# Kernel optimization log

Measured on AMD Instinct MI355X. Metric: run time of the kernel, lower is better.

Reference implementation:

```python
import jax, jax.numpy as jnp
import numpy as np

B, Q, C, K = 2, 300, 80, 300
MH = MW = 128
TH = TW = 320


def setup_inputs() -> dict:
    key = jax.random.key(0)
    k1, k2, k3 = jax.random.split(key, 3)
    pred_logits = jax.random.normal(k1, (B, Q, C), dtype=jnp.float32)
    pred_boxes = jax.random.uniform(k2, (B, Q, 4), dtype=jnp.float32)  # cxcywh in [0,1]
    pred_masks = jax.random.normal(k3, (B, Q, MH, MW), dtype=jnp.float32)
    # fixed target size so resize output shape is static (original uses .item() per image)
    orig_target_sizes = jnp.full((B, 2), 320.0, dtype=jnp.float32)  # (w, h)
    return {
        'pred_logits': pred_logits,
        'pred_boxes': pred_boxes,
        'pred_masks': pred_masks,
        'orig_target_sizes': orig_target_sizes,
        'target_h': TH,
        'target_w': TW,
    }


def reference(pred_logits, pred_boxes, pred_masks, orig_target_sizes, target_h, target_w):
    b, q, c = pred_logits.shape
    # cxcywh -> xyxy
    cx, cy, w, h = jnp.split(pred_boxes, 4, axis=-1)
    boxes_xyxy = jnp.concatenate([cx - 0.5 * w, cy - 0.5 * h, cx + 0.5 * w, cy + 0.5 * h], axis=-1)
    # scale factor [w, h, w, h] per image
    scale_fct = jnp.concatenate([orig_target_sizes, orig_target_sizes], axis=1)[:, None, :]  # [B,1,4]
    boxes_abs = boxes_xyxy * scale_fct  # [B,Q,4]

    # focal-loss path: sigmoid scores, topk over flattened (query, class)
    scores_flat = jax.nn.sigmoid(pred_logits).reshape(b, q * c)
    scores, index_flat = jax.lax.top_k(scores_flat, K)  # [B,K]
    labels = index_flat % c
    query_indices = index_flat // c  # [B,K]

    top_boxes = jnp.take_along_axis(boxes_abs, query_indices[:, :, None], axis=1)  # [B,K,4]
    top_masks = jnp.take_along_axis(pred_masks, query_indices[:, :, None, None], axis=1)  # [B,K,MH,MW]

    # bilinear resize, half-pixel centers == torch align_corners=False
    resized = jax.image.resize(top_masks, (b, K, target_h, target_w), method='linear')
    binary_masks = (jax.nn.sigmoid(resized) > 0.5).astype(jnp.float32)

    return scores, labels, top_boxes, binary_masks
```

## Files before the change

kernel.cpp:

```cpp
#include <hip/hip_runtime.h>
#include <stdint.h>

constexpr int Bq = 2;
constexpr int Qn = 300;
constexpr int Cn = 80;
constexpr int Kn = 300;
constexpr int NFLAT = Qn * Cn;
constexpr int MHs = 128;
constexpr int MWs = 128;
constexpr int THs = 320;
constexpr int TWs = 320;

constexpr int OFF_SCORES = 0;
constexpr int OFF_LABELS = Bq * Kn;
constexpr int OFF_BOXES  = 2 * Bq * Kn;
constexpr int OFF_MASKS  = 2 * Bq * Kn + Bq * Kn * 4;

constexpr int TPB = 1024;
constexpr int EPT = (NFLAT + TPB - 1) / TPB;

typedef float vf4  __attribute__((ext_vector_type(4)));
typedef float uvf4 __attribute__((ext_vector_type(4), aligned(4)));

__global__ __launch_bounds__(TPB) void topk_kernel(
    const float* __restrict__ logits,
    const float* __restrict__ boxes,
    const float* __restrict__ osz,
    float* __restrict__ out,
    int* __restrict__ qidx_ws)
{
    const int b   = blockIdx.x;
    const int tid = threadIdx.x;
    const float* lg = logits + (size_t)b * NFLAT;

    uint32_t key[EPT];
    #pragma unroll
    for (int j = 0; j < EPT; ++j) {
        int idx = j * TPB + tid;
        bool valid = (idx < NFLAT);
        float x = valid ? lg[idx] : 0.0f;
        float s = 1.0f / (1.0f + expf(-x));
        key[j] = valid ? __float_as_uint(s) : 0u;
    }

    __shared__ uint32_t sh_lo, sh_hi;
    __shared__ int sh_cnt, sh_done;
    __shared__ unsigned long long sk[1024];

    if (tid == 0) { sh_lo = 0u; sh_hi = 0xFFFFFFFFu; sh_cnt = 0; sh_done = 0; }
    __syncthreads();

    for (int it = 0; it < 32; ++it) {
        if (sh_done) break;
        uint32_t lo = sh_lo, hi = sh_hi;
        if (hi - lo <= 1) break;
        uint32_t mid = lo + ((hi - lo) >> 1);
        int c = 0;
        #pragma unroll
        for (int j = 0; j < EPT; ++j) c += (key[j] > mid) ? 1 : 0;
        for (int off = 32; off > 0; off >>= 1) c += __shfl_down(c, off);
        if ((tid & 63) == 0 && c) atomicAdd(&sh_cnt, c);
        __syncthreads();
        if (tid == 0) {
            int total = sh_cnt;
            sh_cnt = 0;
            if (total >= Kn) { sh_lo = mid; if (total <= 768) sh_done = 1; }
            else             { sh_hi = mid; }
        }
        __syncthreads();
    }

    const uint32_t T = sh_lo;
    #pragma unroll
    for (int j = 0; j < EPT; ++j) {
        int idx = j * TPB + tid;
        if (idx < NFLAT && key[j] > T) {
            int p = atomicAdd(&sh_cnt, 1);
            if (p < 1024)
                sk[p] = ((unsigned long long)key[j] << 32)
                      | (unsigned long long)(0xFFFFFFFFu - (uint32_t)idx);
        }
    }
    __syncthreads();

    const int n = min(sh_cnt, 1024);
    if (tid < n) {
        unsigned long long my = sk[tid];
        int rank = 0;
        for (int i = 0; i < n; ++i) rank += (sk[i] > my) ? 1 : 0;
        if (rank < Kn) {
            uint32_t idx = 0xFFFFFFFFu - (uint32_t)(my & 0xFFFFFFFFull);
            float score  = __uint_as_float((uint32_t)(my >> 32));
            int label = (int)(idx % (uint32_t)Cn);
            int q     = (int)(idx / (uint32_t)Cn);

            out[OFF_SCORES + b * Kn + rank] = score;
            out[OFF_LABELS + b * Kn + rank] = (float)label;

            const float sw = osz[b * 2 + 0];
            const float sh = osz[b * 2 + 1];
            const float* bx = boxes + ((size_t)(b * Qn + q)) * 4;
            float cx = bx[0], cy = bx[1], w = bx[2], h = bx[3];
            float* ob = out + OFF_BOXES + ((size_t)(b * Kn + rank)) * 4;
            ob[0] = (cx - 0.5f * w) * sw;
            ob[1] = (cy - 0.5f * h) * sh;
            ob[2] = (cx + 0.5f * w) * sw;
            ob[3] = (cy + 0.5f * h) * sh;

            qidx_ws[b * Kn + rank] = q;
        }
    }
}

__global__ __launch_bounds__(320) void resize_kernel(
    const float* __restrict__ masks,
    const int* __restrict__ qidx_ws,
    float* __restrict__ out)
{
    const int blk = blockIdx.x;
    const int bk  = blk >> 2;
    const int s   = blk & 3;
    const int tid = threadIdx.x;
    const int b   = bk / Kn;
    const int q   = qidx_ws[bk];
    const int c   = tid % 80;
    const int rs  = tid / 80;

    const float* M = masks + ((size_t)(b * Qn + q)) * (MHs * MWs);

    int s0;
    {
        float sx0 = fmaf(0.4f, (float)(4 * c), -0.3f);
        int i0 = (int)floorf(sx0);
        s0 = min(max(i0, 0), MWs - 4);
    }
    float W[4][4];
    #pragma unroll
    for (int t = 0; t < 4; ++t) {
        int ox = 4 * c + t;
        float sx = fmaf(0.4f, (float)ox, -0.3f);
        int ix0 = (int)floorf(sx);
        float fr = sx - (float)ix0;
        int ca = max(ix0, 0);
        int cb = min(ix0 + 1, MWs - 1);
        float wa = 1.0f - fr, wb = fr;
        #pragma unroll
        for (int j = 0; j < 4; ++j) {
            float w = 0.0f;
            if (s0 + j == ca) w += wa;
            if (s0 + j == cb) w += wb;
            W[t][j] = w;
        }
    }

    auto hrow = [&](float* hv, int r) {
        uvf4 a = *(const uvf4*)(M + r * MWs + s0);
        #pragma unroll
        for (int t = 0; t < 4; ++t)
            hv[t] = fmaf(W[t][0], a[0],
                    fmaf(W[t][1], a[1],
                    fmaf(W[t][2], a[2], W[t][3] * a[3])));
    };

    float* outm = out + OFF_MASKS + (size_t)bk * (THs * TWs);
    auto emit = [&](int row, float wA, const float* pA, float wB, const float* pB) {
        vf4 o;
        #pragma unroll
        for (int t = 0; t < 4; ++t) {
            float v = fmaf(wA, pA[t], wB * pB[t]);
            o[t] = (v > 0.0f) ? 1.0f : 0.0f;
        }
        __builtin_nontemporal_store(o, (vf4*)(outm + (size_t)row * TWs + 4 * c));
    };

    const int Y0 = 80 * s + 20 * rs;
    const int M0 = Y0 / 5;

    float hA[4], hB[4], hC[4], hD[4];
    hrow(hC, max(2 * M0 - 1, 0));
    hrow(hD, 2 * M0);

    #pragma unroll
    for (int g = 0; g < 4; ++g) {
        #pragma unroll
        for (int t = 0; t < 4; ++t) { hA[t] = hC[t]; hB[t] = hD[t]; }
        const int Mg = M0 + g;
        hrow(hC, 2 * Mg + 1);
        hrow(hD, min(2 * Mg + 2, MHs - 1));

        const int Y = Y0 + 5 * g;
        emit(Y + 0, 0.3f, hA, 0.7f, hB);
        emit(Y + 1, 0.9f, hB, 0.1f, hC);
        emit(Y + 2, 0.5f, hB, 0.5f, hC);
        emit(Y + 3, 0.1f, hB, 0.9f, hC);
        emit(Y + 4, 0.7f, hC, 0.3f, hD);
    }
}

extern "C" void kernel_launch(void* const* d_in, const int* in_sizes, int n_in,
                              void* d_out, int out_size, void* d_ws, size_t ws_size,
                              hipStream_t stream) {
    const float* logits = (const float*)d_in[0];
    const float* boxes  = (const float*)d_in[1];
    const float* masks  = (const float*)d_in[2];
    const float* osz    = (const float*)d_in[3];

    float* out = (float*)d_out;
    int* qidx  = (int*)d_ws;

    topk_kernel<<<Bq, TPB, 0, stream>>>(logits, boxes, osz, out, qidx);
    resize_kernel<<<Bq * Kn * 4, 320, 0, stream>>>(masks, qidx, out);
}
```

Measured before the change: 331.4 us.

## Replace bisection top-k threshold search with single-pass logit histogram

The top-k kernel no longer bisects over sigmoid bit patterns with a barrier per iteration. It builds a 4096-bin shared-memory histogram of the raw logits over [-8, 8), runs a suffix scan to find the bin that holds the k-th element, and applies sigmoid only to the candidates at or above that bin. This cuts the per-iteration reductions and syncs and most exp calls. The risk is that a crowded bin or heavy clamping could push candidates past the 1024-slot buffer; separately, the mask stores become plain stores instead of nontemporal ones.

Measured after the change: 334.4 us. About the same (+0.9%).

```diff
diff --git a/kernel.cpp b/kernel.cpp
--- a/kernel.cpp
+++ b/kernel.cpp
@@ -33,57 +33,82 @@
     const int tid = threadIdx.x;
     const float* lg = logits + (size_t)b * NFLAT;
 
-    uint32_t key[EPT];
+    float xv[EPT];
+    short bn[EPT];
     #pragma unroll
     for (int j = 0; j < EPT; ++j) {
         int idx = j * TPB + tid;
         bool valid = (idx < NFLAT);
-        float x = valid ? lg[idx] : 0.0f;
-        float s = 1.0f / (1.0f + expf(-x));
-        key[j] = valid ? __float_as_uint(s) : 0u;
-    }
-
-    __shared__ uint32_t sh_lo, sh_hi;
-    __shared__ int sh_cnt, sh_done;
+        float x = valid ? lg[idx] : -1e30f;
+        xv[j] = x;
+        int bi = (int)floorf((x + 8.0f) * 256.0f);
+        bn[j] = (short)min(max(bi, 0), 4095);
+        if (!valid) bn[j] = -1;
+    }
+
+    __shared__ int hist[4096];
+    __shared__ int scanA[1024], scanB[1024];
     __shared__ unsigned long long sk[1024];
-
-    if (tid == 0) { sh_lo = 0u; sh_hi = 0xFFFFFFFFu; sh_cnt = 0; sh_done = 0; }
-    __syncthreads();
-
-    for (int it = 0; it < 32; ++it) {
-        if (sh_done) break;
-        uint32_t lo = sh_lo, hi = sh_hi;
-        if (hi - lo <= 1) break;
-        uint32_t mid = lo + ((hi - lo) >> 1);
-        int c = 0;
-        #pragma unroll
-        for (int j = 0; j < EPT; ++j) c += (key[j] > mid) ? 1 : 0;
-        for (int off = 32; off > 0; off >>= 1) c += __shfl_down(c, off);
-        if ((tid & 63) == 0 && c) atomicAdd(&sh_cnt, c);
+    __shared__ int s_cnt, s_seg, s_B;
+
+    {
+        int4* h4 = (int4*)hist;
+        for (int i = tid; i < 4096 / 4; i += TPB) h4[i] = make_int4(0, 0, 0, 0);
+    }
+    if (tid == 0) s_cnt = 0;
+    __syncthreads();
+
+    #pragma unroll
+    for (int j = 0; j < EPT; ++j)
+        if (bn[j] >= 0) atomicAdd(&hist[bn[j]], 1);
+    __syncthreads();
+
+    int sum = hist[4 * tid] + hist[4 * tid + 1] + hist[4 * tid + 2] + hist[4 * tid + 3];
+    scanA[tid] = sum;
+    __syncthreads();
+    int* src = scanA;
+    int* dst = scanB;
+    for (int d = 1; d < 1024; d <<= 1) {
+        int v = src[tid] + ((tid + d < 1024) ? src[tid + d] : 0);
+        dst[tid] = v;
         __syncthreads();
-        if (tid == 0) {
-            int total = sh_cnt;
-            sh_cnt = 0;
-            if (total >= Kn) { sh_lo = mid; if (total <= 768) sh_done = 1; }
-            else             { sh_hi = mid; }
-        }
-        __syncthreads();
-    }
-
-    const uint32_t T = sh_lo;
+        int* t = src; src = dst; dst = t;
+    }
+
+    int sfx  = src[tid];
+    int sfx1 = (tid < 1023) ? src[tid + 1] : 0;
+    if (sfx >= Kn && sfx1 < Kn) s_seg = tid;
+    __syncthreads();
+
+    if (tid == 0) {
+        int t = s_seg;
+        int cumAbove = (t < 1023) ? src[t + 1] : 0;
+        int B = 4 * t;
+        for (int i = 3; i >= 0; --i) {
+            int bin = 4 * t + i;
+            int c = hist[bin];
+            if (cumAbove + c >= Kn) { B = bin; break; }
+            cumAbove += c;
+        }
+        s_B = B;
+    }
+    __syncthreads();
+
+    const int Bv = s_B;
     #pragma unroll
     for (int j = 0; j < EPT; ++j) {
-        int idx = j * TPB + tid;
-        if (idx < NFLAT && key[j] > T) {
-            int p = atomicAdd(&sh_cnt, 1);
+        if ((int)bn[j] >= Bv) {
+            int idx = j * TPB + tid;
+            float s = 1.0f / (1.0f + expf(-xv[j]));
+            int p = atomicAdd(&s_cnt, 1);
             if (p < 1024)
-                sk[p] = ((unsigned long long)key[j] << 32)
+                sk[p] = ((unsigned long long)__float_as_uint(s) << 32)
                       | (unsigned long long)(0xFFFFFFFFu - (uint32_t)idx);
         }
     }
     __syncthreads();
 
-    const int n = min(sh_cnt, 1024);
+    const int n = min(s_cnt, 1024);
     if (tid < n) {
         unsigned long long my = sk[tid];
         int rank = 0;
@@ -170,7 +195,7 @@
             float v = fmaf(wA, pA[t], wB * pB[t]);
             o[t] = (v > 0.0f) ? 1.0f : 0.0f;
         }
-        __builtin_nontemporal_store(o, (vf4*)(outm + (size_t)row * TWs + 4 * c));
+        *(vf4*)(outm + (size_t)row * TWs + 4 * c) = o;
     };
 
     const int Y0 = 80 * s + 20 * rs;
```

## Split top-k into multi-block histogram, threshold, collect and rank kernels

Applied to the files above, without the earlier changes.

Replaces the single-block-per-image bisection top-k with a grid-wide pipeline. A 256-bin logit histogram is built across 47 blocks per image, a threshold bin is picked, candidates are collected by global atomics into a workspace, and a final block ranks them. The aim is to spread the serial 2-block top-k work across many CUs, at the cost of four extra launches plus a memset. The fixed logit-range binning risks more than 1024 candidates, which would silently truncate results. The resize store also switches from nontemporal to a normal store.

New measurement: 345.7 us. 1.04x slower.

```diff
diff --git a/kernel.cpp b/kernel.cpp
--- a/kernel.cpp
+++ b/kernel.cpp
@@ -16,74 +16,89 @@
 constexpr int OFF_BOXES  = 2 * Bq * Kn;
 constexpr int OFF_MASKS  = 2 * Bq * Kn + Bq * Kn * 4;
 
-constexpr int TPB = 1024;
-constexpr int EPT = (NFLAT + TPB - 1) / TPB;
-
 typedef float vf4  __attribute__((ext_vector_type(4)));
 typedef float uvf4 __attribute__((ext_vector_type(4), aligned(4)));
 
-__global__ __launch_bounds__(TPB) void topk_kernel(
-    const float* __restrict__ logits,
-    const float* __restrict__ boxes,
-    const float* __restrict__ osz,
-    float* __restrict__ out,
-    int* __restrict__ qidx_ws)
+constexpr size_t WS_GHIST = 0;
+constexpr size_t WS_CNT   = 2048;
+constexpr size_t WS_THR   = 2064;
+constexpr size_t WS_ZERO_BYTES = 2072;
+constexpr size_t WS_CAND  = 4096;
+constexpr size_t WS_QIDX  = 20480;
+
+__global__ __launch_bounds__(256) void tk_hist(
+    const float* __restrict__ logits, int* __restrict__ ghist)
+{
+    const int b = blockIdx.y;
+    __shared__ int lh[256];
+    lh[threadIdx.x] = 0;
+    __syncthreads();
+    const float* lg = logits + (size_t)b * NFLAT;
+    #pragma unroll
+    for (int j = 0; j < 2; ++j) {
+        int idx = blockIdx.x * 512 + j * 256 + threadIdx.x;
+        if (idx < NFLAT) {
+            float x = lg[idx];
+            int bin = min(max((int)floorf((x + 8.0f) * 16.0f), 0), 255);
+            atomicAdd(&lh[bin], 1);
+        }
+    }
+    __syncthreads();
+    int v = lh[threadIdx.x];
+    if (v) atomicAdd(&ghist[b * 256 + threadIdx.x], v);
+}
+
+__global__ __launch_bounds__(64) void tk_thresh(
+    const int* __restrict__ ghist, int* __restrict__ thr)
+{
+    const int b = blockIdx.x;
+    if (threadIdx.x == 0) {
+        int cum = 0, t = 0;
+        for (int d = 255; d >= 0; --d) {
+            cum += ghist[b * 256 + d];
+            if (cum >= Kn) { t = d; break; }
+        }
+        thr[b] = t;
+    }
+}
+
+__global__ __launch_bounds__(256) void tk_collect(
+    const float* __restrict__ logits, const int* __restrict__ thr,
+    int* __restrict__ cnt, unsigned long long* __restrict__ cand)
+{
+    const int b = blockIdx.y;
+    const int T = thr[b];
+    const float* lg = logits + (size_t)b * NFLAT;
+    #pragma unroll
+    for (int j = 0; j < 2; ++j) {
+        int idx = blockIdx.x * 512 + j * 256 + threadIdx.x;
+        if (idx < NFLAT) {
+            float x = lg[idx];
+            int bin = min(max((int)floorf((x + 8.0f) * 16.0f), 0), 255);
+            if (bin >= T) {
+                float s = 1.0f / (1.0f + expf(-x));
+                int p = atomicAdd(&cnt[b], 1);
+                if (p < 1024)
+                    cand[b * 1024 + p] =
+                        ((unsigned long long)__float_as_uint(s) << 32)
+                      | (unsigned long long)(0xFFFFFFFFu - (uint32_t)idx);
+            }
+        }
+    }
+}
+
+__global__ __launch_bounds__(1024) void tk_rank(
+    const int* __restrict__ cnt, const unsigned long long* __restrict__ cand,
+    const float* __restrict__ boxes, const float* __restrict__ osz,
+    float* __restrict__ out, int* __restrict__ qidx_ws)
 {
     const int b   = blockIdx.x;
     const int tid = threadIdx.x;
-    const float* lg = logits + (size_t)b * NFLAT;
-
-    uint32_t key[EPT];
-    #pragma unroll
-    for (int j = 0; j < EPT; ++j) {
-        int idx = j * TPB + tid;
-        bool valid = (idx < NFLAT);
-        float x = valid ? lg[idx] : 0.0f;
-        float s = 1.0f / (1.0f + expf(-x));
-        key[j] = valid ? __float_as_uint(s) : 0u;
-    }
-
-    __shared__ uint32_t sh_lo, sh_hi;
-    __shared__ int sh_cnt, sh_done;
     __shared__ unsigned long long sk[1024];
-
-    if (tid == 0) { sh_lo = 0u; sh_hi = 0xFFFFFFFFu; sh_cnt = 0; sh_done = 0; }
+    const int n = min(cnt[b], 1024);
+    sk[tid] = (tid < n) ? cand[b * 1024 + tid] : 0ull;
     __syncthreads();
 
-    for (int it = 0; it < 32; ++it) {
-        if (sh_done) break;
-        uint32_t lo = sh_lo, hi = sh_hi;
-        if (hi - lo <= 1) break;
-        uint32_t mid = lo + ((hi - lo) >> 1);
-        int c = 0;
-        #pragma unroll
-        for (int j = 0; j < EPT; ++j) c += (key[j] > mid) ? 1 : 0;
-        for (int off = 32; off > 0; off >>= 1) c += __shfl_down(c, off);
-        if ((tid & 63) == 0 && c) atomicAdd(&sh_cnt, c);
-        __syncthreads();
-        if (tid == 0) {
-            int total = sh_cnt;
-            sh_cnt = 0;
-            if (total >= Kn) { sh_lo = mid; if (total <= 768) sh_done = 1; }
-            else             { sh_hi = mid; }
-        }
-        __syncthreads();
-    }
-
-    const uint32_t T = sh_lo;
-    #pragma unroll
-    for (int j = 0; j < EPT; ++j) {
-        int idx = j * TPB + tid;
-        if (idx < NFLAT && key[j] > T) {
-            int p = atomicAdd(&sh_cnt, 1);
-            if (p < 1024)
-                sk[p] = ((unsigned long long)key[j] << 32)
-                      | (unsigned long long)(0xFFFFFFFFu - (uint32_t)idx);
-        }
-    }
-    __syncthreads();
-
-    const int n = min(sh_cnt, 1024);
     if (tid < n) {
         unsigned long long my = sk[tid];
         int rank = 0;
@@ -170,7 +185,7 @@
             float v = fmaf(wA, pA[t], wB * pB[t]);
             o[t] = (v > 0.0f) ? 1.0f : 0.0f;
         }
-        __builtin_nontemporal_store(o, (vf4*)(outm + (size_t)row * TWs + 4 * c));
+        *(vf4*)(outm + (size_t)row * TWs + 4 * c) = o;
     };
 
     const int Y0 = 80 * s + 20 * rs;
@@ -206,8 +221,19 @@
     const float* osz    = (const float*)d_in[3];
 
     float* out = (float*)d_out;
-    int* qidx  = (int*)d_ws;
-
-    topk_kernel<<<Bq, TPB, 0, stream>>>(logits, boxes, osz, out, qidx);
+    char* ws = (char*)d_ws;
+    int* ghist = (int*)(ws + WS_GHIST);
+    int* cnt   = (int*)(ws + WS_CNT);
+    int* thr   = (int*)(ws + WS_THR);
+    unsigned long long* cand = (unsigned long long*)(ws + WS_CAND);
+    int* qidx  = (int*)(ws + WS_QIDX);
+
+    hipMemsetAsync(ws, 0, WS_ZERO_BYTES, stream);
+
+    dim3 g47(47, Bq);
+    tk_hist<<<g47, 256, 0, stream>>>(logits, ghist);
+    tk_thresh<<<Bq, 64, 0, stream>>>(ghist, thr);
+    tk_collect<<<g47, 256, 0, stream>>>(logits, thr, cnt, cand);
+    tk_rank<<<Bq, 1024, 0, stream>>>(cnt, cand, boxes, osz, out, qidx);
     resize_kernel<<<Bq * Kn * 4, 320, 0, stream>>>(masks, qidx, out);
 }
```
